# Kernel optimization log

Hardware: AMD Instinct MI355X
Metric: run time of the kernel (lower is better)

Reference implementation:

```python
import jax, jax.numpy as jnp
import numpy as np

H, KD, VD = 12, 64, 64  # num_heads, k_dim, v_dim
EPS = 1e-12

def _l2norm(x, axis):
    n = jnp.linalg.norm(x, axis=axis, keepdims=True)
    return x / jnp.maximum(n, EPS)

def setup_inputs() -> dict:
    key = jax.random.key(0)
    ks = jax.random.split(key, 6)
    d1, d2 = 768, 768
    return {
        "x1": jax.random.normal(ks[0], (2048, d1), jnp.float32),
        "x2": jax.random.normal(ks[1], (8192, d2), jnp.float32),
        "Wq": jax.random.normal(ks[2], (H * KD, d1), jnp.float32) * 0.03,
        "Wk": jax.random.normal(ks[3], (H * KD, d2), jnp.float32) * 0.03,
        "Wv": jax.random.normal(ks[4], (H * VD, d2), jnp.float32) * 0.03,
        "Wo": jax.random.normal(ks[5], (d1, H * VD), jnp.float32) * 0.03,
        "invt": 20,
    }

def reference(x1, x2, Wq, Wk, Wv, Wo, invt):
    B1 = x1.shape[0]
    B2 = x2.shape[0]
    # Linear (no bias): y = x @ W.T, then split heads
    q = (x1 @ Wq.T).reshape(B1, H, KD)  # [B1,H,KD]
    k = (x2 @ Wk.T).reshape(B2, H, KD)  # [B2,H,KD]
    v = (x2 @ Wv.T).reshape(B2, H, VD)  # [B2,H,VD]
    # per-head L2 normalization over feature dim (cosine attention)
    q = _l2norm(q, axis=-1)
    k = _l2norm(k, axis=-1)
    attn = jnp.einsum("bhd,nhd->hbn", q, k) * jnp.float32(invt)  # [H,B1,B2]
    attn = jax.nn.softmax(attn, axis=-1)
    out = jnp.einsum("hbn,nhd->bhd", attn, v).reshape(B1, H * VD)
    out = out @ Wo.T  # [B1, in_dim1]
    return _l2norm(out, axis=1)
```

## Files before the change

kernel.cpp:

```cpp
#include <hip/hip_runtime.h>
#include <hip/hip_bf16.h>
#include <math.h>

#define B1 2048
#define B2 8192
#define NH 12
#define DH 64
#define DMODEL 768

typedef __attribute__((ext_vector_type(8))) short short8;
typedef __attribute__((ext_vector_type(4))) float floatx4;
typedef __attribute__((ext_vector_type(8))) unsigned short ushort8;
typedef __attribute__((ext_vector_type(4))) unsigned short ushort4v;

static __device__ __forceinline__ unsigned short f2bf(float f) {
  __bf16 b = (__bf16)f;
  return __builtin_bit_cast(unsigned short, b);
}
static __device__ __forceinline__ float bf2f(unsigned short u) {
  return __builtin_bit_cast(float, ((unsigned)u) << 16);
}

static __device__ __forceinline__ void gload16(const unsigned short* g,
                                               unsigned short* l) {
  __builtin_amdgcn_global_load_lds(
      (const __attribute__((address_space(1))) void*)g,
      (__attribute__((address_space(3))) void*)l, 16, 0, 0);
}

__global__ __launch_bounds__(256) void prep_all(
    const float* __restrict__ x1, unsigned short* __restrict__ x1h,
    const float* __restrict__ x2, unsigned short* __restrict__ x2h,
    const float* __restrict__ Wq, unsigned short* __restrict__ Wqh,
    const float* __restrict__ Wk, unsigned short* __restrict__ Wkh,
    const float* __restrict__ Wv, unsigned short* __restrict__ Wvh,
    const float* __restrict__ Wo, unsigned short* __restrict__ Woh) {
  const int bi = blockIdx.x;
  const float* src;
  unsigned short* hi;
  int lb;
  if (bi < 1536) {
    src = x1; hi = x1h; lb = bi;
  } else if (bi < 7680) {
    src = x2; hi = x2h; lb = bi - 1536;
  } else if (bi < 8256) {
    src = Wq; hi = Wqh; lb = bi - 7680;
  } else if (bi < 8832) {
    src = Wk; hi = Wkh; lb = bi - 8256;
  } else if (bi < 9408) {
    src = Wv; hi = Wvh; lb = bi - 8832;
  } else {
    src = Wo; hi = Woh; lb = bi - 9408;
  }
  const int i = (lb * 256 + threadIdx.x) * 4;
  const float4 v = *(const float4*)&src[i];
  ushort4v h = {f2bf(v.x), f2bf(v.y), f2bf(v.z), f2bf(v.w)};
  *(ushort4v*)&hi[i] = h;
}

template <bool L2N, bool F32OUT>
static __device__ __forceinline__ void gemm_tile(
    const unsigned short* __restrict__ Ahg,
    const unsigned short* __restrict__ Bhg,
    void* __restrict__ Cv, int M, int N, int K, int m0, int n0,
    unsigned short* sAh, unsigned short* sBh) {
  const int tid = threadIdx.x;
  const int wave = tid >> 6;
  const int lane = tid & 63;
  const int wm = wave >> 1;
  const int wn = wave & 1;
  const int n15 = lane & 15;
  const int quad = lane >> 4;
  const int srow = lane >> 2;
  const int cpl = (lane & 3) ^ (srow >> 2);

  floatx4 acc[4][4];
#pragma unroll
  for (int i = 0; i < 4; ++i)
#pragma unroll
    for (int j = 0; j < 4; ++j) acc[i][j] = (floatx4){0.f, 0.f, 0.f, 0.f};

  for (int k0 = 0; k0 < K; k0 += 32) {
    __syncthreads();
#pragma unroll
    for (int jj = 0; jj < 2; ++jj) {
      const int j = wave * 2 + jj;
      const int row = j * 16 + srow;
      const size_t goffA = (size_t)(m0 + row) * K + k0 + cpl * 8;
      const size_t goffB = (size_t)(n0 + row) * K + k0 + cpl * 8;
      gload16(Ahg + goffA, &sAh[j * 512]);
      gload16(Bhg + goffB, &sBh[j * 512]);
    }
    __syncthreads();

    short8 afh[4];
#pragma unroll
    for (int mt = 0; mt < 4; ++mt) {
      const int row = wm * 64 + mt * 16 + n15;
      const int off = row * 32 + ((quad ^ (n15 >> 2)) << 3);
      afh[mt] = *(const short8*)&sAh[off];
    }
#pragma unroll
    for (int nt = 0; nt < 4; ++nt) {
      const int row = wn * 64 + nt * 16 + n15;
      const int off = row * 32 + ((quad ^ (n15 >> 2)) << 3);
      const short8 bfh = *(const short8*)&sBh[off];
#pragma unroll
      for (int mt = 0; mt < 4; ++mt)
        acc[mt][nt] = __builtin_amdgcn_mfma_f32_16x16x32_bf16(afh[mt], bfh, acc[mt][nt], 0, 0, 0);
    }
  }

#pragma unroll
  for (int mt = 0; mt < 4; ++mt) {
    float scalev[4] = {1.f, 1.f, 1.f, 1.f};
    if constexpr (L2N) {
#pragma unroll
      for (int rr = 0; rr < 4; ++rr) {
        float ss = 0.f;
#pragma unroll
        for (int nt = 0; nt < 4; ++nt) ss += acc[mt][nt][rr] * acc[mt][nt][rr];
        ss += __shfl_xor(ss, 1, 64);
        ss += __shfl_xor(ss, 2, 64);
        ss += __shfl_xor(ss, 4, 64);
        ss += __shfl_xor(ss, 8, 64);
        scalev[rr] = 1.0f / fmaxf(sqrtf(ss), 1e-12f);
      }
    }
#pragma unroll
    for (int nt = 0; nt < 4; ++nt) {
#pragma unroll
      for (int rr = 0; rr < 4; ++rr) {
        const int row = m0 + wm * 64 + mt * 16 + quad * 4 + rr;
        const int col = n0 + wn * 64 + nt * 16 + n15;
        const float v = acc[mt][nt][rr] * scalev[rr];
        if constexpr (F32OUT)
          ((float*)Cv)[(size_t)row * N + col] = v;
        else
          ((unsigned short*)Cv)[(size_t)row * N + col] = f2bf(v);
      }
    }
  }
}

__global__ __launch_bounds__(256) void qkv_proj(
    const unsigned short* __restrict__ x1h,
    const unsigned short* __restrict__ Wqh,
    const unsigned short* __restrict__ x2h,
    const unsigned short* __restrict__ Wkh,
    const unsigned short* __restrict__ Wvh,
    unsigned short* __restrict__ qbf, unsigned short* __restrict__ kbf,
    unsigned short* __restrict__ vtbf) {
  __shared__ __align__(16) unsigned short sAh[4096], sBh[4096];
  const int bi = blockIdx.x;
  if (bi < 96) {
    gemm_tile<true, false>(x1h, Wqh, qbf, B1, DMODEL, DMODEL,
                           (bi / 6) * 128, (bi % 6) * 128, sAh, sBh);
  } else if (bi < 480) {
    const int b = bi - 96;
    gemm_tile<true, false>(x2h, Wkh, kbf, B2, DMODEL, DMODEL,
                           (b / 6) * 128, (b % 6) * 128, sAh, sBh);
  } else {
    const int b = bi - 480;
    gemm_tile<false, false>(Wvh, x2h, vtbf, DMODEL, B2, DMODEL,
                            (b / 64) * 128, (b % 64) * 128, sAh, sBh);
  }
}

#define KC 128
#define KSPLIT 2
#define NCH (B2 / KSPLIT / KC)
#define PSTR 68

__global__ __launch_bounds__(256, 3) void attn_mfma(
    const unsigned short* __restrict__ qb, const unsigned short* __restrict__ kb,
    const unsigned short* __restrict__ vt, float* __restrict__ aoacc,
    float* __restrict__ lacc, const int* __restrict__ invt_p) {
  __shared__ __align__(16) unsigned short smem[25088];
  unsigned short* Psl = smem + 16384;

  const int bid = blockIdx.x;
  const int swz = (bid & 7) * 96 + (bid >> 3);
  const int zz = swz / 384;
  const int rem = swz - zz * 384;
  const int h = rem >> 5;
  const int q0 = (rem & 31) * 64;

  const float c2 = (float)invt_p[0] * 1.4426950408889634f;
  const int tid = threadIdx.x;
  const int wave = tid >> 6;
  const int lane = tid & 63;
  const int qsub = wave >> 1;
  const int ksub = wave & 1;
  const int n15 = lane & 15;
  const int quad = lane >> 4;
  const int kz0 = zz * (B2 / KSPLIT);

  unsigned short* Ps = &Psl[wave * 32 * PSTR];

  short8 qf[2][2];
#pragma unroll
  for (int qt = 0; qt < 2; ++qt)
#pragma unroll
    for (int ks = 0; ks < 2; ++ks) {
      const int qrow = q0 + qsub * 32 + qt * 16 + n15;
      qf[qt][ks] = *(const short8*)&qb[(size_t)qrow * DMODEL + h * DH + ks * 32 + quad * 8];
    }

  floatx4 oacc[2][4];
#pragma unroll
  for (int qt = 0; qt < 2; ++qt)
#pragma unroll
    for (int nt = 0; nt < 4; ++nt) oacc[qt][nt] = (floatx4){0.f, 0.f, 0.f, 0.f};
  float lsum[2] = {0.f, 0.f};

  const unsigned short* kbp = kb + (size_t)kz0 * DMODEL + h * DH;
  const unsigned short* vbp = vt + (size_t)(h * DH) * B2 + kz0;

  ushort8 kr[4];
#pragma unroll
  for (int i = 0; i < 4; ++i) {
    const int s = i * 256 + tid;
    const int key = s >> 3, cpk = s & 7, chk = cpk ^ (key & 7);
    kr[i] = *(const ushort8*)&kbp[(size_t)key * DMODEL + chk * 8];
  }
#pragma unroll
  for (int i = 0; i < 4; ++i) {
    const int s = i * 256 + tid;
    const int key = s >> 3, cpk = s & 7;
    *(ushort8*)&smem[key * 64 + cpk * 8] = kr[i];
  }
#pragma unroll
  for (int i = 0; i < 4; ++i) {
    const int s = i * 256 + tid;
    const int key = s >> 3, cpk = s & 7, chk = cpk ^ (key & 7);
    kr[i] = *(const ushort8*)&kbp[(size_t)(KC + key) * DMODEL + chk * 8];
  }
  __syncthreads();

  for (int c = 0; c < NCH; ++c) {
    unsigned short* Kb = &smem[(c & 1) * 8192];
    unsigned short* Kn = &smem[((c + 1) & 1) * 8192];
    const unsigned short* vc_ = vbp + c * KC;

    ushort8 vr[8];
#pragma unroll
    for (int ks = 0; ks < 2; ++ks)
#pragma unroll
      for (int nt = 0; nt < 4; ++nt)
        vr[ks * 4 + nt] = *(const ushort8*)&vc_[
            (size_t)(nt * 16 + n15) * B2 + (ksub * 8 + ks * 4 + quad) * 8];

    if (c + 1 < NCH) {
#pragma unroll
      for (int i = 0; i < 4; ++i) {
        const int s = i * 256 + tid;
        const int key = s >> 3, cpk = s & 7;
        *(ushort8*)&Kn[key * 64 + cpk * 8] = kr[i];
      }
      if (c + 2 < NCH) {
        const unsigned short* k2 = kbp + (size_t)(c + 2) * KC * DMODEL;
#pragma unroll
        for (int i = 0; i < 4; ++i) {
          const int s = i * 256 + tid;
          const int key = s >> 3, cpk = s & 7, chk = cpk ^ (key & 7);
          kr[i] = *(const ushort8*)&k2[(size_t)key * DMODEL + chk * 8];
        }
      }
    }

#pragma unroll
    for (int kt = 0; kt < 4; ++kt) {
      floatx4 s0 = {0.f, 0.f, 0.f, 0.f}, s1 = {0.f, 0.f, 0.f, 0.f};
#pragma unroll
      for (int ks = 0; ks < 2; ++ks) {
        const int key = ksub * 64 + kt * 16 + n15;
        const int cp = (ks * 4 + quad) ^ (n15 & 7);
        const short8 kf = *(const short8*)&Kb[key * 64 + cp * 8];
        s0 = __builtin_amdgcn_mfma_f32_16x16x32_bf16(kf, qf[0][ks], s0, 0, 0, 0);
        s1 = __builtin_amdgcn_mfma_f32_16x16x32_bf16(kf, qf[1][ks], s1, 0, 0, 0);
      }
      ushort4v p0, p1;
#pragma unroll
      for (int r = 0; r < 4; ++r) {
        const float e0 = exp2f(fmaf(s0[r], c2, -c2));
        const float e1 = exp2f(fmaf(s1[r], c2, -c2));
        lsum[0] += e0;
        lsum[1] += e1;
        p0[r] = f2bf(e0);
        p1[r] = f2bf(e1);
      }
      *(ushort4v*)&Ps[(0 * 16 + n15) * PSTR + kt * 16 + quad * 4] = p0;
      *(ushort4v*)&Ps[(1 * 16 + n15) * PSTR + kt * 16 + quad * 4] = p1;
    }

#pragma unroll
    for (int ks = 0; ks < 2; ++ks) {
      short8 pa[2];
#pragma unroll
      for (int qt = 0; qt < 2; ++qt)
        pa[qt] = *(const short8*)&Ps[(qt * 16 + n15) * PSTR + ks * 32 + quad * 8];
#pragma unroll
      for (int nt = 0; nt < 4; ++nt) {
        const short8 vf = __builtin_bit_cast(short8, vr[ks * 4 + nt]);
        oacc[0][nt] = __builtin_amdgcn_mfma_f32_16x16x32_bf16(pa[0], vf, oacc[0][nt], 0, 0, 0);
        oacc[1][nt] = __builtin_amdgcn_mfma_f32_16x16x32_bf16(pa[1], vf, oacc[1][nt], 0, 0, 0);
      }
    }

    __syncthreads();
  }

#pragma unroll
  for (int qt = 0; qt < 2; ++qt) {
    float v = lsum[qt];
    v += __shfl_xor(v, 16, 64);
    v += __shfl_xor(v, 32, 64);
    lsum[qt] = v;
  }

  float* aoz = aoacc + (size_t)zz * B1 * DMODEL;
  float* lz = lacc + (size_t)zz * B1 * NH;

  __syncthreads();
  float* Osc = (float*)smem;
  float* lsc = Osc + 4096;
  if (ksub == 1) {
#pragma unroll
    for (int qt = 0; qt < 2; ++qt)
#pragma unroll
      for (int nt = 0; nt < 4; ++nt)
#pragma unroll
        for (int r = 0; r < 4; ++r) {
          const int row = qsub * 32 + qt * 16 + quad * 4 + r;
          Osc[row * 64 + nt * 16 + n15] = oacc[qt][nt][r];
        }
    if (quad == 0) {
      lsc[qsub * 32 + n15] = lsum[0];
      lsc[qsub * 32 + 16 + n15] = lsum[1];
    }
  }
  __syncthreads();
  if (ksub == 0) {
#pragma unroll
    for (int qt = 0; qt < 2; ++qt)
#pragma unroll
      for (int nt = 0; nt < 4; ++nt)
#pragma unroll
        for (int r = 0; r < 4; ++r) {
          const int row = qsub * 32 + qt * 16 + quad * 4 + r;
          const float v = oacc[qt][nt][r] + Osc[row * 64 + nt * 16 + n15];
          aoz[(size_t)(q0 + row) * DMODEL + h * DH + nt * 16 + n15] = v;
        }
    if (quad == 0) {
      lz[(size_t)(q0 + qsub * 32 + n15) * NH + h] = lsum[0] + lsc[qsub * 32 + n15];
      lz[(size_t)(q0 + qsub * 32 + 16 + n15) * NH + h] =
          lsum[1] + lsc[qsub * 32 + 16 + n15];
    }
  }
}

__global__ __launch_bounds__(256) void wo_proj(
    const float* __restrict__ aoacc, const float* __restrict__ lacc,
    const unsigned short* __restrict__ Woh, float* __restrict__ woout) {
  __shared__ __align__(16) unsigned short sAh[4096], sBh[4096];
  const int bi = blockIdx.x;
  const int m0 = (bi / 6) * 128;
  const int n0 = (bi % 6) * 128;
  const int tid = threadIdx.x;
  const int wave = tid >> 6;
  const int lane = tid & 63;
  const int wm = wave >> 1;
  const int wn = wave & 1;
  const int n15 = lane & 15;
  const int quad = lane >> 4;
  const int srow = lane >> 2;
  const int cpl = (lane & 3) ^ (srow >> 2);

  const float* ao1 = aoacc + (size_t)B1 * DMODEL;
  const float* la1 = lacc + (size_t)B1 * NH;

  floatx4 acc[4][4];
#pragma unroll
  for (int i = 0; i < 4; ++i)
#pragma unroll
    for (int j = 0; j < 4; ++j) acc[i][j] = (floatx4){0.f, 0.f, 0.f, 0.f};

  for (int k0 = 0; k0 < DMODEL; k0 += 32) {
    __syncthreads();
#pragma unroll
    for (int jj = 0; jj < 2; ++jj) {
      const int j = wave * 2 + jj;
      const int row = j * 16 + srow;
      const size_t ga = (size_t)(m0 + row) * DMODEL + k0 + cpl * 8;
      const float4 a0 = *(const float4*)&aoacc[ga];
      const float4 a1 = *(const float4*)&aoacc[ga + 4];
      const float4 b0 = *(const float4*)&ao1[ga];
      const float4 b1 = *(const float4*)&ao1[ga + 4];
      const int head = (k0 + cpl * 8) >> 6;
      const float lsum = lacc[(m0 + row) * NH + head] + la1[(m0 + row) * NH + head];
      const float inv = 1.0f / lsum;
      ushort8 ah = {f2bf((a0.x + b0.x) * inv), f2bf((a0.y + b0.y) * inv),
                    f2bf((a0.z + b0.z) * inv), f2bf((a0.w + b0.w) * inv),
                    f2bf((a1.x + b1.x) * inv), f2bf((a1.y + b1.y) * inv),
                    f2bf((a1.z + b1.z) * inv), f2bf((a1.w + b1.w) * inv)};
      *(ushort8*)&sAh[j * 512 + lane * 8] = ah;
      gload16(Woh + (size_t)(n0 + row) * DMODEL + k0 + cpl * 8, &sBh[j * 512]);
    }
    __syncthreads();

    short8 afh[4];
#pragma unroll
    for (int mt = 0; mt < 4; ++mt) {
      const int row = wm * 64 + mt * 16 + n15;
      afh[mt] = *(const short8*)&sAh[row * 32 + ((quad ^ (n15 >> 2)) << 3)];
    }
#pragma unroll
    for (int nt = 0; nt < 4; ++nt) {
      const int row = wn * 64 + nt * 16 + n15;
      const short8 bfh = *(const short8*)&sBh[row * 32 + ((quad ^ (n15 >> 2)) << 3)];
#pragma unroll
      for (int mt = 0; mt < 4; ++mt)
        acc[mt][nt] = __builtin_amdgcn_mfma_f32_16x16x32_bf16(afh[mt], bfh, acc[mt][nt], 0, 0, 0);
    }
  }

#pragma unroll
  for (int mt = 0; mt < 4; ++mt)
#pragma unroll
    for (int nt = 0; nt < 4; ++nt)
#pragma unroll
      for (int rr = 0; rr < 4; ++rr) {
        const int row = m0 + wm * 64 + mt * 16 + quad * 4 + rr;
        const int col = n0 + wn * 64 + nt * 16 + n15;
        woout[(size_t)row * DMODEL + col] = acc[mt][nt][rr];
      }
}

__global__ __launch_bounds__(256) void l2norm_rows768_out(
    const float* __restrict__ x, float* __restrict__ out) {
  const int row = blockIdx.x;
  const float* xr = &x[(size_t)row * DMODEL];
  float ss = 0.0f;
  float vals[3];
#pragma unroll
  for (int i = 0; i < 3; ++i) {
    vals[i] = xr[threadIdx.x + i * 256];
    ss += vals[i] * vals[i];
  }
#pragma unroll
  for (int off = 32; off > 0; off >>= 1) ss += __shfl_xor(ss, off, 64);
  __shared__ float ws[4];
  if ((threadIdx.x & 63) == 0) ws[threadIdx.x >> 6] = ss;
  __syncthreads();
  const float tot = ws[0] + ws[1] + ws[2] + ws[3];
  const float sc = 1.0f / fmaxf(sqrtf(tot), 1e-12f);
  float* orow = &out[(size_t)row * DMODEL];
#pragma unroll
  for (int i = 0; i < 3; ++i) orow[threadIdx.x + i * 256] = vals[i] * sc;
}

extern "C" void kernel_launch(void* const* d_in, const int* in_sizes, int n_in,
                              void* d_out, int out_size, void* d_ws,
                              size_t ws_size, hipStream_t stream) {
  const float* x1 = (const float*)d_in[0];
  const float* x2 = (const float*)d_in[1];
  const float* Wq = (const float*)d_in[2];
  const float* Wk = (const float*)d_in[3];
  const float* Wv = (const float*)d_in[4];
  const float* Wo = (const float*)d_in[5];
  const int* invt = (const int*)d_in[6];
  float* outp = (float*)d_out;

  char* ws = (char*)d_ws;
  unsigned short* x1h = (unsigned short*)(ws + 0);
  unsigned short* x2h = (unsigned short*)(ws + 6291456);
  unsigned short* Wqh = (unsigned short*)(ws + 31457280);
  unsigned short* Wkh = (unsigned short*)(ws + 33816576);
  unsigned short* Wvh = (unsigned short*)(ws + 36175872);
  unsigned short* Woh = (unsigned short*)(ws + 37355520);
  unsigned short* q_bf = (unsigned short*)(ws + 38535168);
  unsigned short* k_bf = (unsigned short*)(ws + 41680896);
  float* aoacc = (float*)(ws + 0);
  float* lacc = (float*)(ws + 32636928);
  unsigned short* vt_bf = (unsigned short*)(ws + 18874368);
  float* woout = (float*)(ws + 12582912);

  prep_all<<<9984, 256, 0, stream>>>(x1, x1h, x2, x2h, Wq, Wqh,
                                     Wk, Wkh, Wv, Wvh, Wo, Woh);
  qkv_proj<<<864, 256, 0, stream>>>(x1h, Wqh, x2h, Wkh, Wvh,
                                    q_bf, k_bf, vt_bf);
  attn_mfma<<<768, 256, 0, stream>>>(q_bf, k_bf, vt_bf, aoacc, lacc, invt);
  wo_proj<<<96, 256, 0, stream>>>(aoacc, lacc, Woh, woout);
  l2norm_rows768_out<<<B1, 256, 0, stream>>>(woout, outp);
}
```

Baseline: 292.3 us.

## Fuse fp32-to-bf16 conversion into projection GEMM tile loads, drop prep kernel

Removes the separate prep_all kernel that converted inputs and weights to bf16. The QKV and output projection GEMMs now read fp32 directly, convert in registers and store bf16 to shared memory, with register prefetch of the next K-slice. This saves one kernel launch and a full write-then-read of the bf16 copies. In exchange the GEMMs load twice the bytes per tile, redo the conversion for every tile that reads the same data, and lose the asynchronous global-to-LDS load path.

```diff
diff --git a/kernel.cpp b/kernel.cpp
--- a/kernel.cpp
+++ b/kernel.cpp
@@ -17,9 +17,6 @@
   __bf16 b = (__bf16)f;
   return __builtin_bit_cast(unsigned short, b);
 }
-static __device__ __forceinline__ float bf2f(unsigned short u) {
-  return __builtin_bit_cast(float, ((unsigned)u) << 16);
-}
 
 static __device__ __forceinline__ void gload16(const unsigned short* g,
                                                unsigned short* l) {
@@ -28,40 +25,9 @@
       (__attribute__((address_space(3))) void*)l, 16, 0, 0);
 }
 
-__global__ __launch_bounds__(256) void prep_all(
-    const float* __restrict__ x1, unsigned short* __restrict__ x1h,
-    const float* __restrict__ x2, unsigned short* __restrict__ x2h,
-    const float* __restrict__ Wq, unsigned short* __restrict__ Wqh,
-    const float* __restrict__ Wk, unsigned short* __restrict__ Wkh,
-    const float* __restrict__ Wv, unsigned short* __restrict__ Wvh,
-    const float* __restrict__ Wo, unsigned short* __restrict__ Woh) {
-  const int bi = blockIdx.x;
-  const float* src;
-  unsigned short* hi;
-  int lb;
-  if (bi < 1536) {
-    src = x1; hi = x1h; lb = bi;
-  } else if (bi < 7680) {
-    src = x2; hi = x2h; lb = bi - 1536;
-  } else if (bi < 8256) {
-    src = Wq; hi = Wqh; lb = bi - 7680;
-  } else if (bi < 8832) {
-    src = Wk; hi = Wkh; lb = bi - 8256;
-  } else if (bi < 9408) {
-    src = Wv; hi = Wvh; lb = bi - 8832;
-  } else {
-    src = Wo; hi = Woh; lb = bi - 9408;
-  }
-  const int i = (lb * 256 + threadIdx.x) * 4;
-  const float4 v = *(const float4*)&src[i];
-  ushort4v h = {f2bf(v.x), f2bf(v.y), f2bf(v.z), f2bf(v.w)};
-  *(ushort4v*)&hi[i] = h;
-}
-
 template <bool L2N, bool F32OUT>
-static __device__ __forceinline__ void gemm_tile(
-    const unsigned short* __restrict__ Ahg,
-    const unsigned short* __restrict__ Bhg,
+static __device__ __forceinline__ void gemm_tile_f32(
+    const float* __restrict__ Ag, const float* __restrict__ Bg,
     void* __restrict__ Cv, int M, int N, int K, int m0, int n0,
     unsigned short* sAh, unsigned short* sBh) {
   const int tid = threadIdx.x;
@@ -80,16 +46,43 @@
 #pragma unroll
     for (int j = 0; j < 4; ++j) acc[i][j] = (floatx4){0.f, 0.f, 0.f, 0.f};
 
+  float4 ar[2][2], br[2][2];
+#pragma unroll
+  for (int jj = 0; jj < 2; ++jj) {
+    const int row = (wave * 2 + jj) * 16 + srow;
+    const size_t ga = (size_t)(m0 + row) * K + cpl * 8;
+    const size_t gb = (size_t)(n0 + row) * K + cpl * 8;
+    ar[jj][0] = *(const float4*)&Ag[ga];
+    ar[jj][1] = *(const float4*)&Ag[ga + 4];
+    br[jj][0] = *(const float4*)&Bg[gb];
+    br[jj][1] = *(const float4*)&Bg[gb + 4];
+  }
+
   for (int k0 = 0; k0 < K; k0 += 32) {
     __syncthreads();
 #pragma unroll
     for (int jj = 0; jj < 2; ++jj) {
       const int j = wave * 2 + jj;
-      const int row = j * 16 + srow;
-      const size_t goffA = (size_t)(m0 + row) * K + k0 + cpl * 8;
-      const size_t goffB = (size_t)(n0 + row) * K + k0 + cpl * 8;
-      gload16(Ahg + goffA, &sAh[j * 512]);
-      gload16(Bhg + goffB, &sBh[j * 512]);
+      const float4 a0 = ar[jj][0], a1 = ar[jj][1];
+      const float4 b0 = br[jj][0], b1 = br[jj][1];
+      ushort8 ah = {f2bf(a0.x), f2bf(a0.y), f2bf(a0.z), f2bf(a0.w),
+                    f2bf(a1.x), f2bf(a1.y), f2bf(a1.z), f2bf(a1.w)};
+      ushort8 bh = {f2bf(b0.x), f2bf(b0.y), f2bf(b0.z), f2bf(b0.w),
+                    f2bf(b1.x), f2bf(b1.y), f2bf(b1.z), f2bf(b1.w)};
+      *(ushort8*)&sAh[j * 512 + lane * 8] = ah;
+      *(ushort8*)&sBh[j * 512 + lane * 8] = bh;
+    }
+    if (k0 + 32 < K) {
+#pragma unroll
+      for (int jj = 0; jj < 2; ++jj) {
+        const int row = (wave * 2 + jj) * 16 + srow;
+        const size_t ga = (size_t)(m0 + row) * K + (k0 + 32) + cpl * 8;
+        const size_t gb = (size_t)(n0 + row) * K + (k0 + 32) + cpl * 8;
+        ar[jj][0] = *(const float4*)&Ag[ga];
+        ar[jj][1] = *(const float4*)&Ag[ga + 4];
+        br[jj][0] = *(const float4*)&Bg[gb];
+        br[jj][1] = *(const float4*)&Bg[gb + 4];
+      }
     }
     __syncthreads();
 
@@ -144,26 +137,24 @@
 }
 
 __global__ __launch_bounds__(256) void qkv_proj(
-    const unsigned short* __restrict__ x1h,
-    const unsigned short* __restrict__ Wqh,
-    const unsigned short* __restrict__ x2h,
-    const unsigned short* __restrict__ Wkh,
-    const unsigned short* __restrict__ Wvh,
+    const float* __restrict__ x1, const float* __restrict__ Wq,
+    const float* __restrict__ x2, const float* __restrict__ Wk,
+    const float* __restrict__ Wv,
     unsigned short* __restrict__ qbf, unsigned short* __restrict__ kbf,
     unsigned short* __restrict__ vtbf) {
   __shared__ __align__(16) unsigned short sAh[4096], sBh[4096];
   const int bi = blockIdx.x;
   if (bi < 96) {
-    gemm_tile<true, false>(x1h, Wqh, qbf, B1, DMODEL, DMODEL,
-                           (bi / 6) * 128, (bi % 6) * 128, sAh, sBh);
+    gemm_tile_f32<true, false>(x1, Wq, qbf, B1, DMODEL, DMODEL,
+                               (bi / 6) * 128, (bi % 6) * 128, sAh, sBh);
   } else if (bi < 480) {
     const int b = bi - 96;
-    gemm_tile<true, false>(x2h, Wkh, kbf, B2, DMODEL, DMODEL,
-                           (b / 6) * 128, (b % 6) * 128, sAh, sBh);
+    gemm_tile_f32<true, false>(x2, Wk, kbf, B2, DMODEL, DMODEL,
+                               (b / 6) * 128, (b % 6) * 128, sAh, sBh);
   } else {
     const int b = bi - 480;
-    gemm_tile<false, false>(Wvh, x2h, vtbf, DMODEL, B2, DMODEL,
-                            (b / 64) * 128, (b % 64) * 128, sAh, sBh);
+    gemm_tile_f32<false, false>(Wv, x2, vtbf, DMODEL, B2, DMODEL,
+                                (b / 64) * 128, (b % 64) * 128, sAh, sBh);
   }
 }
 
@@ -362,7 +353,7 @@
 
 __global__ __launch_bounds__(256) void wo_proj(
     const float* __restrict__ aoacc, const float* __restrict__ lacc,
-    const unsigned short* __restrict__ Woh, float* __restrict__ woout) {
+    const float* __restrict__ Wo, float* __restrict__ woout) {
   __shared__ __align__(16) unsigned short sAh[4096], sBh[4096];
   const int bi = blockIdx.x;
   const int m0 = (bi / 6) * 128;
@@ -405,7 +396,12 @@
                     f2bf((a1.x + b1.x) * inv), f2bf((a1.y + b1.y) * inv),
                     f2bf((a1.z + b1.z) * inv), f2bf((a1.w + b1.w) * inv)};
       *(ushort8*)&sAh[j * 512 + lane * 8] = ah;
-      gload16(Woh + (size_t)(n0 + row) * DMODEL + k0 + cpl * 8, &sBh[j * 512]);
+      const size_t gb = (size_t)(n0 + row) * DMODEL + k0 + cpl * 8;
+      const float4 w0 = *(const float4*)&Wo[gb];
+      const float4 w1 = *(const float4*)&Wo[gb + 4];
+      ushort8 bh = {f2bf(w0.x), f2bf(w0.y), f2bf(w0.z), f2bf(w0.w),
+                    f2bf(w1.x), f2bf(w1.y), f2bf(w1.z), f2bf(w1.w)};
+      *(ushort8*)&sBh[j * 512 + lane * 8] = bh;
     }
     __syncthreads();
 
@@ -473,24 +469,15 @@
   float* outp = (float*)d_out;
 
   char* ws = (char*)d_ws;
-  unsigned short* x1h = (unsigned short*)(ws + 0);
-  unsigned short* x2h = (unsigned short*)(ws + 6291456);
-  unsigned short* Wqh = (unsigned short*)(ws + 31457280);
-  unsigned short* Wkh = (unsigned short*)(ws + 33816576);
-  unsigned short* Wvh = (unsigned short*)(ws + 36175872);
-  unsigned short* Woh = (unsigned short*)(ws + 37355520);
+  float* aoacc = (float*)(ws + 0);
+  float* woout = (float*)(ws + 12582912);
+  unsigned short* vt_bf = (unsigned short*)(ws + 18874368);
+  float* lacc = (float*)(ws + 32636928);
   unsigned short* q_bf = (unsigned short*)(ws + 38535168);
   unsigned short* k_bf = (unsigned short*)(ws + 41680896);
-  float* aoacc = (float*)(ws + 0);
-  float* lacc = (float*)(ws + 32636928);
-  unsigned short* vt_bf = (unsigned short*)(ws + 18874368);
-  float* woout = (float*)(ws + 12582912);
-
-  prep_all<<<9984, 256, 0, stream>>>(x1, x1h, x2, x2h, Wq, Wqh,
-                                     Wk, Wkh, Wv, Wvh, Wo, Woh);
-  qkv_proj<<<864, 256, 0, stream>>>(x1h, Wqh, x2h, Wkh, Wvh,
-                                    q_bf, k_bf, vt_bf);
+
+  qkv_proj<<<864, 256, 0, stream>>>(x1, Wq, x2, Wk, Wv, q_bf, k_bf, vt_bf);
   attn_mfma<<<768, 256, 0, stream>>>(q_bf, k_bf, vt_bf, aoacc, lacc, invt);
-  wo_proj<<<96, 256, 0, stream>>>(aoacc, lacc, Woh, woout);
+  wo_proj<<<96, 256, 0, stream>>>(aoacc, lacc, Wo, woout);
   l2norm_rows768_out<<<B1, 256, 0, stream>>>(woout, outp);
 }
```

Result: no change. 291.1 us (-0.4%).
